# Kernel tuning notes

Hardware: AMD Instinct MI355X
Metric: run time of the kernel (lower is better)

The kernel has to match this reference:

```python
import jax, jax.numpy as jnp
import numpy as np

NUM_HEADS = 16
D_MODEL = 1024
MASK_VALUE = -1000000.0


def setup_inputs() -> dict:
    key = jax.random.key(0)
    ks = jax.random.split(key, 8)
    B, S, D = 2, 2048, D_MODEL
    scale = 1.0 / np.sqrt(D)
    return {
        "queries": jax.random.normal(ks[0], (B, S, D), dtype=jnp.float32),
        "keys": jax.random.normal(ks[1], (B, S, D), dtype=jnp.float32),
        "values": jax.random.normal(ks[2], (B, S, D), dtype=jnp.float32),
        "valid_lens": jax.random.randint(ks[3], (B,), 1, S + 1),
        # Linear weights stored as (in, out); no bias (bias=False)
        "Wq": jax.random.normal(ks[4], (D, D), dtype=jnp.float32) * scale,
        "Wk": jax.random.normal(ks[5], (D, D), dtype=jnp.float32) * scale,
        "Wv": jax.random.normal(ks[6], (D, D), dtype=jnp.float32) * scale,
        "Wo": jax.random.normal(ks[7], (D, D), dtype=jnp.float32) * scale,
    }


def reference(queries, keys, values, valid_lens, Wq, Wk, Wv, Wo):
    B, Sq, D = queries.shape
    Sk = keys.shape[1]
    H = NUM_HEADS
    hd = D // H

    def split_heads(x, S):
        # (B, S, D) -> (B, H, S, hd)
        return x.reshape(B, S, H, hd).transpose(0, 2, 1, 3)

    q = split_heads(queries @ Wq, Sq)
    k = split_heads(keys @ Wk, Sk)
    v = split_heads(values @ Wv, Sk)

    # Faithful to original bug: d_k = queries.size(0) after head-flattening = B*H
    scale = 1.0 / jnp.sqrt(jnp.float32(B * H))
    scores = jnp.einsum("bhqd,bhkd->bhqk", q, k) * scale  # (B,H,Sq,Sk)

    # sequence_mask over last dim, per batch row (valid_lens repeated per head)
    mask = jnp.arange(Sk)[None, None, None, :] < valid_lens[:, None, None, None]
    scores = jnp.where(mask, scores, MASK_VALUE)
    attn = jax.nn.softmax(scores, axis=-1)

    out = jnp.einsum("bhqk,bhkd->bhqd", attn, v)  # (B,H,Sq,hd)
    out = out.transpose(0, 2, 1, 3).reshape(B, Sq, D)
    return out @ Wo
```

## Files before the change

kernel.cpp:

```cpp
#include <hip/hip_runtime.h>
#include <stdint.h>

#define NH 16
#define SEQ 2048
#define DMODEL 1024
#define HD 64
#define NBATCH 2
#define MTOT (NBATCH * SEQ)
#define QSCALE 0.17677669529663687f
#define LOG2E 1.4426950408889634f

typedef __bf16 bf16x8 __attribute__((ext_vector_type(8)));
typedef float f32x4 __attribute__((ext_vector_type(4)));
typedef float f32x16 __attribute__((ext_vector_type(16)));
typedef unsigned uint4v __attribute__((ext_vector_type(4)));

__device__ __forceinline__ unsigned short bf16u(float x) {
  unsigned u = __builtin_bit_cast(unsigned, x);
  u += 0x7fffu + ((u >> 16) & 1u);
  return (unsigned short)(u >> 16);
}

__device__ __forceinline__ float exp2_fast(float x) {
  float r;
  asm("v_exp_f32 %0, %1" : "=v"(r) : "v"(x));
  return r;
}

__device__ __forceinline__ f32x4 mfma16(bf16x8 a, bf16x8 b, f32x4 c) {
  return __builtin_amdgcn_mfma_f32_16x16x32_bf16(a, b, c, 0, 0, 0);
}
__device__ __forceinline__ f32x16 mfma32(bf16x8 a, bf16x8 b, f32x16 c) {
  return __builtin_amdgcn_mfma_f32_32x32x16_bf16(a, b, c, 0, 0, 0);
}

__device__ __forceinline__ void gl16(const void* g, void* l) {
  __builtin_amdgcn_global_load_lds(
      (const __attribute__((address_space(1))) void*)g,
      (__attribute__((address_space(3))) void*)l, 16, 0, 0);
}

__device__ __forceinline__ unsigned cvtpk(float a, float b) {
  unsigned r;
  asm("v_cvt_pk_bf16_f32 %0, %1, %2" : "=v"(r) : "v"(a), "v"(b));
  return r;
}


__global__ __launch_bounds__(256) void prep_kernel(
    const float* __restrict__ x0, const float* __restrict__ x1,
    const float* __restrict__ x2, unsigned short* __restrict__ o0,
    unsigned short* __restrict__ o1, unsigned short* __restrict__ o2,
    const float* __restrict__ w0, const float* __restrict__ w1,
    const float* __restrict__ w2, const float* __restrict__ w3,
    unsigned short* __restrict__ t0, unsigned short* __restrict__ t1,
    unsigned short* __restrict__ t2, unsigned short* __restrict__ t3) {
  const int id = blockIdx.x;
  if (id < 1536) {
    const int src = id >> 9, blk = id & 511;
    const float* s = (src == 0) ? x0 : (src == 1) ? x1 : x2;
    unsigned short* d = (src == 0) ? o0 : (src == 1) ? o1 : o2;
    const int n4 = MTOT * DMODEL / 4;
    for (int i = blk * 256 + threadIdx.x; i < n4; i += 512 * 256) {
      float4 f = reinterpret_cast<const float4*>(s)[i];
      ushort4 u;
      u.x = bf16u(f.x); u.y = bf16u(f.y); u.z = bf16u(f.z); u.w = bf16u(f.w);
      reinterpret_cast<ushort4*>(d)[i] = u;
    }
  } else {
    __shared__ float tile[64][65];
    const int id2 = id - 1536;
    const int wsel = id2 >> 8, tl = id2 & 255;
    const float* w = (wsel == 0) ? w0 : (wsel == 1) ? w1
                     : (wsel == 2) ? w2 : w3;
    unsigned short* t = (wsel == 0) ? t0 : (wsel == 1) ? t1
                        : (wsel == 2) ? t2 : t3;
    const float scl = (wsel == 0) ? QSCALE * LOG2E : 1.0f;
    int n0 = (tl & 15) * 64, k0 = (tl >> 4) * 64;
    int tx = threadIdx.x & 63, ty = threadIdx.x >> 6;
#pragma unroll
    for (int i = 0; i < 16; ++i) {
      int kk = ty * 16 + i;
      tile[kk][tx] = w[(k0 + kk) * DMODEL + n0 + tx];
    }
    __syncthreads();
#pragma unroll
    for (int i = 0; i < 16; ++i) {
      int nn = ty * 16 + i;
      t[(n0 + nn) * DMODEL + k0 + tx] = bf16u(tile[tx][nn] * scl);
    }
  }
}

__global__ __launch_bounds__(256) void gemm_qkv_kernel(
    const unsigned short* __restrict__ xq, const unsigned short* __restrict__ xk,
    const unsigned short* __restrict__ xv,
    const unsigned short* __restrict__ wq, const unsigned short* __restrict__ wk,
    const unsigned short* __restrict__ wv,
    unsigned short* __restrict__ qb, unsigned short* __restrict__ kb,
    unsigned short* __restrict__ vp) {
  __shared__ unsigned short lA[3][128 * 32];
  __shared__ unsigned short lB[3][128 * 32];
  const int z = blockIdx.z;
  const unsigned short* A = (z == 0) ? xq : (z == 1) ? xk : xv;
  const unsigned short* Wt = (z == 0) ? wq : (z == 1) ? wk : wv;
  unsigned short* outb = (z == 0) ? qb : (z == 1) ? kb : vp;

  const int tid = threadIdx.x;
  const int lane = tid & 63, wid = tid >> 6;
  const int wr = wid >> 1, wc = wid & 1;
  const int m0 = blockIdx.x * 128, n0 = blockIdx.y * 128;
  const int lm = lane & 15, lg = lane >> 4;

  auto stage = [&](int buf, int kt) {
#pragma unroll
    for (int i = 0; i < 2; ++i) {
      int c = tid + i * 256;
      int row = c >> 2, cb = c & 3;
      int scb = cb ^ ((row >> 1) & 3);
      gl16(A + (m0 + row) * DMODEL + kt * 32 + scb * 8, (char*)lA[buf] + c * 16);
      gl16(Wt + (n0 + row) * DMODEL + kt * 32 + scb * 8, (char*)lB[buf] + c * 16);
    }
  };

  f32x4 acc[4][4] = {};
  stage(0, 0);
  stage(1, 1);

  const int NKT = DMODEL / 32;
  for (int kt = 0; kt < NKT; ++kt) {
    if (kt == NKT - 1) {
      asm volatile("s_waitcnt vmcnt(0)" ::: "memory");
    } else {
      asm volatile("s_waitcnt vmcnt(4)" ::: "memory");
    }
    __builtin_amdgcn_sched_barrier(0);
    __builtin_amdgcn_s_barrier();
    __builtin_amdgcn_sched_barrier(0);

    if (kt + 2 < NKT) stage((kt + 2) % 3, kt + 2);

    const int cur = kt % 3;
    bf16x8 af[4], bfr[4];
#pragma unroll
    for (int x = 0; x < 4; ++x) {
      int rowA = wr * 64 + x * 16 + lm;
      int rowB = wc * 64 + x * 16 + lm;
      int uA = lg ^ ((rowA >> 1) & 3);
      int uB = lg ^ ((rowB >> 1) & 3);
      af[x] = *reinterpret_cast<const bf16x8*>(
          (const char*)&lA[cur][0] + rowA * 64 + uA * 16);
      bfr[x] = *reinterpret_cast<const bf16x8*>(
          (const char*)&lB[cur][0] + rowB * 64 + uB * 16);
    }
#pragma unroll
    for (int mi = 0; mi < 4; ++mi)
#pragma unroll
      for (int ni = 0; ni < 4; ++ni)
        acc[mi][ni] = mfma16(af[mi], bfr[ni], acc[mi][ni]);
  }

  const int lg2 = lane >> 4;
#pragma unroll
  for (int mi = 0; mi < 4; ++mi)
#pragma unroll
    for (int ni = 0; ni < 4; ++ni) {
      int col = n0 + wc * 64 + ni * 16 + lm;
#pragma unroll
      for (int r = 0; r < 4; ++r) {
        int row = m0 + wr * 64 + mi * 16 + lg2 * 4 + r;
        int b = row >> 11, s = row & (SEQ - 1);
        int h = col >> 6, d = col & (HD - 1);
        unsigned short val = bf16u(acc[mi][ni][r]);
        if (z != 2) {
          outb[(((b * NH + h) * SEQ + s) * HD + d)] = val;
        } else {
          int kt2 = s >> 6, rem6 = s & 63;
          int ff = rem6 >> 4, rem = rem6 & 15;
          int jj = (rem & 3) | ((rem >> 3) << 2);
          int hh = (rem >> 2) & 1;
          size_t pidx =
              (((((size_t)(b * NH + h) * 32 + kt2) * 2 + (d >> 5)) * 4 + ff) * 64
               + hh * 32 + (d & 31)) * 8 + jj;
          outb[pidx] = val;
        }
      }
    }
}

__global__ __launch_bounds__(256) void gemm_out_kernel(
    const unsigned short* __restrict__ A, const unsigned short* __restrict__ Wt,
    float* __restrict__ outf) {
  __shared__ unsigned short lA[3][128 * 32];
  __shared__ unsigned short lB[3][64 * 32];
  const int tid = threadIdx.x;
  const int lane = tid & 63, wr = tid >> 6;
  const int m0 = blockIdx.x * 128, n0 = blockIdx.y * 64;
  const int lm = lane & 15, lg = lane >> 4;

  auto stage = [&](int buf, int kt) {
#pragma unroll
    for (int i = 0; i < 2; ++i) {
      int c = tid + i * 256;
      int row = c >> 2, cb = c & 3;
      int scb = cb ^ ((row >> 1) & 3);
      gl16(A + (m0 + row) * DMODEL + kt * 32 + scb * 8, (char*)lA[buf] + c * 16);
    }
    int c = tid;
    int row = c >> 2, cb = c & 3;
    int scb = cb ^ ((row >> 1) & 3);
    gl16(Wt + (n0 + row) * DMODEL + kt * 32 + scb * 8, (char*)lB[buf] + c * 16);
  };

  f32x4 acc[2][4] = {};
  stage(0, 0);
  stage(1, 1);

  const int NKT = DMODEL / 32;
  for (int kt = 0; kt < NKT; ++kt) {
    if (kt == NKT - 1) {
      asm volatile("s_waitcnt vmcnt(0)" ::: "memory");
    } else {
      asm volatile("s_waitcnt vmcnt(3)" ::: "memory");
    }
    __builtin_amdgcn_sched_barrier(0);
    __builtin_amdgcn_s_barrier();
    __builtin_amdgcn_sched_barrier(0);

    if (kt + 2 < NKT) stage((kt + 2) % 3, kt + 2);

    const int cur = kt % 3;
    bf16x8 af[2], bfr[4];
#pragma unroll
    for (int x = 0; x < 2; ++x) {
      int rowA = wr * 32 + x * 16 + lm;
      int uA = lg ^ ((rowA >> 1) & 3);
      af[x] = *reinterpret_cast<const bf16x8*>(
          (const char*)&lA[cur][0] + rowA * 64 + uA * 16);
    }
#pragma unroll
    for (int x = 0; x < 4; ++x) {
      int rowB = x * 16 + lm;
      int uB = lg ^ ((rowB >> 1) & 3);
      bfr[x] = *reinterpret_cast<const bf16x8*>(
          (const char*)&lB[cur][0] + rowB * 64 + uB * 16);
    }
#pragma unroll
    for (int mi = 0; mi < 2; ++mi)
#pragma unroll
      for (int ni = 0; ni < 4; ++ni)
        acc[mi][ni] = mfma16(af[mi], bfr[ni], acc[mi][ni]);
  }

  const int lg2 = lane >> 4;
#pragma unroll
  for (int mi = 0; mi < 2; ++mi)
#pragma unroll
    for (int ni = 0; ni < 4; ++ni) {
      int col = n0 + ni * 16 + lm;
#pragma unroll
      for (int r = 0; r < 4; ++r) {
        int row = m0 + wr * 32 + mi * 16 + lg2 * 4 + r;
        outf[row * DMODEL + col] = acc[mi][ni][r];
      }
    }
}

__global__ __launch_bounds__(256, 2) void attn17_kernel(
    const unsigned short* __restrict__ qb, const unsigned short* __restrict__ kb,
    const unsigned short* __restrict__ vp, const int* __restrict__ vlens,
    unsigned short* __restrict__ ao) {
  __shared__ char klds[4][2][8192];
  const int lane = threadIdx.x & 63;
  const int w = threadIdx.x >> 6;
  const int qi = lane & 31, hi = lane >> 5;
  const int wid = blockIdx.x * 4 + w;
  const int bhi = wid & 31;
  const int chunk = wid >> 5;
  const int b = bhi & 1, h = bhi >> 1;
  const int bh = b * NH + h;
  const int s0w = chunk * 32;
  const int vlen = vlens[b];
  const int nkt = (vlen + 63) >> 6;

  const unsigned short* kbase = kb + bh * SEQ * HD;
  const unsigned short* vpb = vp + (size_t)bh * 32 * 2 * 4 * 64 * 8;

  const unsigned short* qrow = qb + (bh * SEQ + s0w + qi) * HD;
  bf16x8 qf[4];
#pragma unroll
  for (int ks = 0; ks < 4; ++ks)
    qf[ks] = *reinterpret_cast<const bf16x8*>(qrow + ks * 16 + hi * 8);

  f32x16 oacc[2] = {};
  float m = -3e38f, l = 0.f;

  const int srow = lane >> 3;
  const int scol8 = (lane & 7) ^ (srow & 7);
  auto stageK = [&](int buf, int kt) {
    int k0 = kt * 64;
    char* dst = &klds[w][buf][0];
#pragma unroll
    for (int i = 0; i < 8; ++i)
      gl16(kbase + (size_t)(k0 + i * 8 + srow) * HD + scol8 * 8,
           dst + i * 1024);
  };

  auto readK = [&](bf16x8* kr, int buf) {
    const char* base = &klds[w][buf][0];
#pragma unroll
    for (int kb2 = 0; kb2 < 2; ++kb2)
#pragma unroll
      for (int ks = 0; ks < 4; ++ks) {
        int row = kb2 * 32 + qi;
        int off = row * 128 + ((ks * 32 + hi * 16) ^ ((qi & 7) << 4));
        kr[kb2 * 4 + ks] = *reinterpret_cast<const bf16x8*>(base + off);
      }
  };

  auto body = [&](int t, int buf) {
    const int k0 = t * 64;
    const bool lastt = (t == nkt - 1);

    asm volatile("s_waitcnt vmcnt(0)" ::: "memory");
    __builtin_amdgcn_sched_barrier(0);

    bf16x8 kr[8];
    readK(kr, buf);

    f32x16 s0 = {}, s1 = {};
    __builtin_amdgcn_s_setprio(1);
#pragma unroll
    for (int ks = 0; ks < 4; ++ks) s0 = mfma32(kr[ks], qf[ks], s0);
#pragma unroll
    for (int ks = 0; ks < 4; ++ks) s1 = mfma32(kr[4 + ks], qf[ks], s1);
    __builtin_amdgcn_s_setprio(0);

    if (!lastt) stageK(buf ^ 1, t + 1);

    const unsigned short* vtile = vpb + (size_t)t * 2 * 4 * 64 * 8;
    bf16x8 vr[8];
#pragma unroll
    for (int db = 0; db < 2; ++db)
#pragma unroll
      for (int f = 0; f < 4; ++f)
        vr[db * 4 + f] = *reinterpret_cast<const bf16x8*>(
            vtile + ((db * 4 + f) * 64 + lane) * 8);

    if (lastt) {
#pragma unroll
      for (int r = 0; r < 16; ++r) {
        int key = k0 + (r & 3) + 8 * (r >> 2) + 4 * hi;
        if (key >= vlen) s0[r] = -1.4426950e6f;
        if (key + 32 >= vlen) s1[r] = -1.4426950e6f;
      }
    }

    float mx8[8];
#pragma unroll
    for (int i = 0; i < 8; ++i)
      mx8[i] = fmaxf(fmaxf(s0[i], s0[i + 8]), fmaxf(s1[i], s1[i + 8]));
#pragma unroll
    for (int st = 4; st; st >>= 1)
#pragma unroll
      for (int i = 0; i < st; ++i) mx8[i] = fmaxf(mx8[i], mx8[i + st]);
    float mx = fmaxf(mx8[0], __shfl_xor(mx8[0], 32, 64));
    float mn = fmaxf(m, mx);
    float sf = exp2_fast(m - mn);
    m = mn;

#pragma unroll
    for (int r = 0; r < 16; ++r) s0[r] = exp2_fast(s0[r] - mn);
#pragma unroll
    for (int r = 0; r < 16; ++r) s1[r] = exp2_fast(s1[r] - mn);
    float sm8[8];
#pragma unroll
    for (int i = 0; i < 8; ++i)
      sm8[i] = (s0[i] + s0[i + 8]) + (s1[i] + s1[i + 8]);
#pragma unroll
    for (int st = 4; st; st >>= 1)
#pragma unroll
      for (int i = 0; i < st; ++i) sm8[i] += sm8[i + st];
    float ps = sm8[0] + __shfl_xor(sm8[0], 32, 64);
    l = l * sf + ps;
#pragma unroll
    for (int db = 0; db < 2; ++db) oacc[db] *= sf;

    bf16x8 pf[4];
    auto packP = [&](const f32x16& s, bf16x8* out) {
#pragma unroll
      for (int f = 0; f < 2; ++f) {
        uint4v wv;
#pragma unroll
        for (int k2 = 0; k2 < 4; ++k2)
          wv[k2] = cvtpk(s[f * 8 + k2 * 2], s[f * 8 + k2 * 2 + 1]);
        out[f] = __builtin_bit_cast(bf16x8, wv);
      }
    };
    packP(s0, pf);
    packP(s1, pf + 2);

    __builtin_amdgcn_s_setprio(1);
#pragma unroll
    for (int db = 0; db < 2; ++db)
#pragma unroll
      for (int f = 0; f < 4; ++f)
        oacc[db] = mfma32(vr[db * 4 + f], pf[f], oacc[db]);
    __builtin_amdgcn_s_setprio(0);
  };

  stageK(0, 0);
  for (int t = 0; t < nkt; ++t) body(t, t & 1);

  const float linv = 1.0f / l;
#pragma unroll
  for (int db = 0; db < 2; ++db)
#pragma unroll
    for (int rq = 0; rq < 4; ++rq) {
      ushort4 o;
      o.x = bf16u(oacc[db][rq * 4 + 0] * linv);
      o.y = bf16u(oacc[db][rq * 4 + 1] * linv);
      o.z = bf16u(oacc[db][rq * 4 + 2] * linv);
      o.w = bf16u(oacc[db][rq * 4 + 3] * linv);
      int d = db * 32 + 8 * rq + 4 * hi;
      *reinterpret_cast<ushort4*>(
          ao + (b * SEQ + s0w + qi) * DMODEL + h * HD + d) = o;
    }
}

extern "C" void kernel_launch(void* const* d_in, const int* in_sizes, int n_in,
                              void* d_out, int out_size, void* d_ws, size_t ws_size,
                              hipStream_t stream) {
  (void)in_sizes; (void)n_in; (void)out_size; (void)ws_size;
  const float* q = (const float*)d_in[0];
  const float* k = (const float*)d_in[1];
  const float* v = (const float*)d_in[2];
  const int* vlens = (const int*)d_in[3];
  const float* Wq = (const float*)d_in[4];
  const float* Wk = (const float*)d_in[5];
  const float* Wv = (const float*)d_in[6];
  const float* Wo = (const float*)d_in[7];
  float* out = (float*)d_out;

  char* ws = (char*)d_ws;
  const size_t MB = 1u << 20;
  unsigned short* xq = (unsigned short*)(ws + 0 * MB);
  unsigned short* xk = (unsigned short*)(ws + 8 * MB);
  unsigned short* xv = (unsigned short*)(ws + 16 * MB);
  unsigned short* wqt = (unsigned short*)(ws + 24 * MB);
  unsigned short* wkt = (unsigned short*)(ws + 26 * MB);
  unsigned short* wvt = (unsigned short*)(ws + 28 * MB);
  unsigned short* wot = (unsigned short*)(ws + 30 * MB);
  unsigned short* qb = (unsigned short*)(ws + 32 * MB);
  unsigned short* kb = (unsigned short*)(ws + 40 * MB);
  unsigned short* vpk = (unsigned short*)(ws + 48 * MB);
  unsigned short* ao = (unsigned short*)(ws + 56 * MB);

  prep_kernel<<<dim3(2560), 256, 0, stream>>>(q, k, v, xq, xk, xv,
                                              Wq, Wk, Wv, Wo,
                                              wqt, wkt, wvt, wot);
  gemm_qkv_kernel<<<dim3(32, 8, 3), 256, 0, stream>>>(xq, xk, xv,
                                                      wqt, wkt, wvt,
                                                      qb, kb, vpk);
  attn17_kernel<<<dim3(512), 256, 0, stream>>>(qb, kb, vpk, vlens, ao);
  gemm_out_kernel<<<dim3(32, 16), 256, 0, stream>>>(ao, wot, out);
}
```

Measured before the change: 105.7 us.

## Pre-pack K in MFMA fragment layout and load it directly into registers

The QKV GEMM now writes K in a packed per-lane fragment layout, matching how V was already packed. The attention kernel drops its LDS staging of K and loads K fragments straight from global memory into registers, prefetching the next tile into a ping-pong register pair. This removes LDS traffic, the explicit vmcnt wait and the LDS footprint that limited occupancy. In exchange it uses more VGPRs for the double-buffered K, and occupancy is no longer pinned by the launch-bounds minimum-blocks hint.

```diff
diff --git a/kernel.cpp b/kernel.cpp
--- a/kernel.cpp
+++ b/kernel.cpp
@@ -97,14 +97,14 @@
     const unsigned short* __restrict__ xv,
     const unsigned short* __restrict__ wq, const unsigned short* __restrict__ wk,
     const unsigned short* __restrict__ wv,
-    unsigned short* __restrict__ qb, unsigned short* __restrict__ kb,
+    unsigned short* __restrict__ qb, unsigned short* __restrict__ kp,
     unsigned short* __restrict__ vp) {
   __shared__ unsigned short lA[3][128 * 32];
   __shared__ unsigned short lB[3][128 * 32];
   const int z = blockIdx.z;
   const unsigned short* A = (z == 0) ? xq : (z == 1) ? xk : xv;
   const unsigned short* Wt = (z == 0) ? wq : (z == 1) ? wk : wv;
-  unsigned short* outb = (z == 0) ? qb : (z == 1) ? kb : vp;
+  unsigned short* outb = (z == 0) ? qb : (z == 1) ? kp : vp;
 
   const int tid = threadIdx.x;
   const int lane = tid & 63, wid = tid >> 6;
@@ -172,8 +172,15 @@
         int b = row >> 11, s = row & (SEQ - 1);
         int h = col >> 6, d = col & (HD - 1);
         unsigned short val = bf16u(acc[mi][ni][r]);
-        if (z != 2) {
+        if (z == 0) {
           outb[(((b * NH + h) * SEQ + s) * HD + d)] = val;
+        } else if (z == 1) {
+          int kt2 = s >> 6, kb2 = (s >> 5) & 1, qi2 = s & 31;
+          int ks2 = d >> 4, hh = (d >> 3) & 1, jj = d & 7;
+          size_t pidx =
+              (((((size_t)(b * NH + h) * 32 + kt2) * 2 + kb2) * 4 + ks2) * 64
+               + hh * 32 + qi2) * 8 + jj;
+          outb[pidx] = val;
         } else {
           int kt2 = s >> 6, rem6 = s & 63;
           int ff = rem6 >> 4, rem = rem6 & 15;
@@ -266,11 +273,10 @@
     }
 }
 
-__global__ __launch_bounds__(256, 2) void attn17_kernel(
-    const unsigned short* __restrict__ qb, const unsigned short* __restrict__ kb,
+__global__ __launch_bounds__(256) void attn21_kernel(
+    const unsigned short* __restrict__ qb, const unsigned short* __restrict__ kp,
     const unsigned short* __restrict__ vp, const int* __restrict__ vlens,
     unsigned short* __restrict__ ao) {
-  __shared__ char klds[4][2][8192];
   const int lane = threadIdx.x & 63;
   const int w = threadIdx.x >> 6;
   const int qi = lane & 31, hi = lane >> 5;
@@ -283,7 +289,7 @@
   const int vlen = vlens[b];
   const int nkt = (vlen + 63) >> 6;
 
-  const unsigned short* kbase = kb + bh * SEQ * HD;
+  const unsigned short* kpb = kp + (size_t)bh * 32 * 2 * 4 * 64 * 8;
   const unsigned short* vpb = vp + (size_t)bh * 32 * 2 * 4 * 64 * 8;
 
   const unsigned short* qrow = qb + (bh * SEQ + s0w + qi) * HD;
@@ -295,57 +301,34 @@
   f32x16 oacc[2] = {};
   float m = -3e38f, l = 0.f;
 
-  const int srow = lane >> 3;
-  const int scol8 = (lane & 7) ^ (srow & 7);
-  auto stageK = [&](int buf, int kt) {
-    int k0 = kt * 64;
-    char* dst = &klds[w][buf][0];
-#pragma unroll
-    for (int i = 0; i < 8; ++i)
-      gl16(kbase + (size_t)(k0 + i * 8 + srow) * HD + scol8 * 8,
-           dst + i * 1024);
+  auto loadK = [&](bf16x8* kr, int t) {
+    const unsigned short* kt = kpb + (size_t)t * 2 * 4 * 64 * 8;
+#pragma unroll
+    for (int f = 0; f < 8; ++f)
+      kr[f] = *reinterpret_cast<const bf16x8*>(kt + (f * 64 + lane) * 8);
   };
-
-  auto readK = [&](bf16x8* kr, int buf) {
-    const char* base = &klds[w][buf][0];
-#pragma unroll
-    for (int kb2 = 0; kb2 < 2; ++kb2)
-#pragma unroll
-      for (int ks = 0; ks < 4; ++ks) {
-        int row = kb2 * 32 + qi;
-        int off = row * 128 + ((ks * 32 + hi * 16) ^ ((qi & 7) << 4));
-        kr[kb2 * 4 + ks] = *reinterpret_cast<const bf16x8*>(base + off);
-      }
+  auto loadV = [&](bf16x8* vr, int t) {
+    const unsigned short* vt = vpb + (size_t)t * 2 * 4 * 64 * 8;
+#pragma unroll
+    for (int f = 0; f < 8; ++f)
+      vr[f] = *reinterpret_cast<const bf16x8*>(vt + (f * 64 + lane) * 8);
   };
 
-  auto body = [&](int t, int buf) {
+  auto body = [&](int t, bf16x8* krCur, bf16x8* krNext) {
     const int k0 = t * 64;
     const bool lastt = (t == nkt - 1);
 
-    asm volatile("s_waitcnt vmcnt(0)" ::: "memory");
-    __builtin_amdgcn_sched_barrier(0);
-
-    bf16x8 kr[8];
-    readK(kr, buf);
+    bf16x8 vr[8];
+    loadV(vr, t);
+    if (!lastt) loadK(krNext, t + 1);
 
     f32x16 s0 = {}, s1 = {};
     __builtin_amdgcn_s_setprio(1);
 #pragma unroll
-    for (int ks = 0; ks < 4; ++ks) s0 = mfma32(kr[ks], qf[ks], s0);
-#pragma unroll
-    for (int ks = 0; ks < 4; ++ks) s1 = mfma32(kr[4 + ks], qf[ks], s1);
+    for (int ks = 0; ks < 4; ++ks) s0 = mfma32(krCur[ks], qf[ks], s0);
+#pragma unroll
+    for (int ks = 0; ks < 4; ++ks) s1 = mfma32(krCur[4 + ks], qf[ks], s1);
     __builtin_amdgcn_s_setprio(0);
-
-    if (!lastt) stageK(buf ^ 1, t + 1);
-
-    const unsigned short* vtile = vpb + (size_t)t * 2 * 4 * 64 * 8;
-    bf16x8 vr[8];
-#pragma unroll
-    for (int db = 0; db < 2; ++db)
-#pragma unroll
-      for (int f = 0; f < 4; ++f)
-        vr[db * 4 + f] = *reinterpret_cast<const bf16x8*>(
-            vtile + ((db * 4 + f) * 64 + lane) * 8);
 
     if (lastt) {
 #pragma unroll
@@ -409,8 +392,13 @@
     __builtin_amdgcn_s_setprio(0);
   };
 
-  stageK(0, 0);
-  for (int t = 0; t < nkt; ++t) body(t, t & 1);
+  bf16x8 krA[8], krB[8];
+  loadK(krA, 0);
+  for (int t = 0; t < nkt; t += 2) {
+    body(t, krA, krB);
+    if (t + 1 >= nkt) break;
+    body(t + 1, krB, krA);
+  }
 
   const float linv = 1.0f / l;
 #pragma unroll
@@ -452,7 +440,7 @@
   unsigned short* wvt = (unsigned short*)(ws + 28 * MB);
   unsigned short* wot = (unsigned short*)(ws + 30 * MB);
   unsigned short* qb = (unsigned short*)(ws + 32 * MB);
-  unsigned short* kb = (unsigned short*)(ws + 40 * MB);
+  unsigned short* kpk = (unsigned short*)(ws + 40 * MB);
   unsigned short* vpk = (unsigned short*)(ws + 48 * MB);
   unsigned short* ao = (unsigned short*)(ws + 56 * MB);
 
@@ -461,7 +449,7 @@
                                               wqt, wkt, wvt, wot);
   gemm_qkv_kernel<<<dim3(32, 8, 3), 256, 0, stream>>>(xq, xk, xv,
                                                       wqt, wkt, wvt,
-                                                      qb, kb, vpk);
-  attn17_kernel<<<dim3(512), 256, 0, stream>>>(qb, kb, vpk, vlens, ao);
+                                                      qb, kpk, vpk);
+  attn21_kernel<<<dim3(512), 256, 0, stream>>>(qb, kpk, vpk, vlens, ao);
   gemm_out_kernel<<<dim3(32, 16), 256, 0, stream>>>(ao, wot, out);
 }
```

Result: slower. 135.6 us (+28.3%).
